# Kernel tuning notes

Measured on AMD Instinct MI355X. Metric: run time of the kernel, lower is better.

## Reference

```python
import jax, jax.numpy as jnp
import numpy as np

B = 65536
HIDDEN = 200
K = 10          # num codewords == codeword dim (NearestEmbed(k, emb_size=k))
GROUPS = HIDDEN // K  # 20 sub-vectors of dim K per sample


def setup_inputs() -> dict:
    key = jax.random.key(0)
    ks = jax.random.split(key, 10)
    s = 0.05  # small init scale
    return {
        "x": jax.random.uniform(ks[0], (B, 784), dtype=jnp.float32),
        "W1": jax.random.normal(ks[1], (400, 784), dtype=jnp.float32) * s,
        "b1": jnp.zeros((400,), dtype=jnp.float32),
        "W2": jax.random.normal(ks[2], (HIDDEN, 400), dtype=jnp.float32) * s,
        "b2": jnp.zeros((HIDDEN,), dtype=jnp.float32),
        "W3": jax.random.normal(ks[3], (400, HIDDEN), dtype=jnp.float32) * s,
        "b3": jnp.zeros((400,), dtype=jnp.float32),
        "W4": jax.random.normal(ks[4], (784, 400), dtype=jnp.float32) * s,
        "b4": jnp.zeros((784,), dtype=jnp.float32),
        "codebook": jax.random.normal(ks[5], (K, K), dtype=jnp.float32),  # (n_codes, code_dim)
    }


def _quantize(z, codebook):
    # z: (B, K, GROUPS) -- quantize each length-K column vector to nearest codeword.
    v = jnp.transpose(z, (0, 2, 1))                       # (B, G, K)
    d2 = (jnp.sum(v * v, -1, keepdims=True)
          - 2.0 * jnp.einsum('bgk,ck->bgc', v, codebook)
          + jnp.sum(codebook * codebook, -1))             # (B, G, C)
    idx = jnp.argmin(d2, axis=-1)                         # (B, G)
    q = codebook[idx]                                     # (B, G, K) gather
    return jnp.transpose(q, (0, 2, 1)), idx               # (B, K, G)


def reference(x, W1, b1, W2, b2, W3, b3, W4, b4, codebook):
    # encode
    h1 = jax.nn.relu(x @ W1.T + b1)                       # (B, 400)
    z_e_flat = h1 @ W2.T + b2                             # (B, 200)
    z_e = z_e_flat.reshape(B, K, GROUPS)                  # (B, 10, 20)

    # z_q: straight-through quantization, codebook grad stopped (weight_sg=True)
    q, _ = _quantize(z_e, codebook)
    z_q = (z_e + jax.lax.stop_gradient(q - z_e)).reshape(B, HIDDEN)

    # emb: quantize detached z_e; gradient flows only to codebook via gather
    q2, _ = _quantize(jax.lax.stop_gradient(z_e), codebook)
    emb = q2.reshape(B, HIDDEN)

    # decode (original uses tanh on the output)
    h3 = jax.nn.relu(z_q @ W3.T + b3)                     # (B, 400)
    recon = jnp.tanh(h3 @ W4.T + b4)                      # (B, 784)
    return recon, z_e, emb
```

## Files before the change

### kernel.cpp

```cpp
#include <hip/hip_runtime.h>
#include <hip/hip_bf16.h>

#define NB   65536
#define KD   10
#define NG   20
#define NH   200
#define NH1  400
#define NIN  784

#define TAU 3e-4

using short8 = __attribute__((ext_vector_type(8))) short;
using f32x4  = __attribute__((ext_vector_type(4))) float;

__device__ inline float bf2f(unsigned short u) {
  union { unsigned int i; float f; } x; x.i = ((unsigned int)u) << 16; return x.f;
}
__device__ inline unsigned short f2bf(float v) {
  __hip_bfloat16 b = __float2bfloat16(v);
  return *reinterpret_cast<unsigned short*>(&b);
}
__device__ inline void split2(float v, unsigned short& h, unsigned short& l) {
  union { float f; unsigned int i; } u; u.f = v;
  const unsigned int hbits = u.i & 0xffff0000u;
  h = (unsigned short)(hbits >> 16);
  union { unsigned int i; float f; } w; w.i = hbits;
  l = f2bf(v - w.f);
}
__device__ inline void gload_lds16(const void* g, void* l) {
  __builtin_amdgcn_global_load_lds(
      (const __attribute__((address_space(1))) unsigned int*)g,
      (__attribute__((address_space(3))) unsigned int*)l, 16, 0, 0);
}

#define KSWZ(lane) ((((lane) & 3) ^ (((lane) >> 3) & 3)) * 8)
#define CSW(lane)  (((((lane) >> 4) ^ (((lane) >> 1) & 3))) * 8)

__global__ __launch_bounds__(256) void gemm1_fused(
    const float* __restrict__ xf,
    const unsigned short* __restrict__ Bhi, const unsigned short* __restrict__ Blo,
    const float* __restrict__ bias,
    unsigned short* __restrict__ Ohi, unsigned short* __restrict__ Olo)
{
  __shared__ __align__(16) short As_hi[2][128][32];
  __shared__ __align__(16) short As_lo[2][128][32];
  __shared__ __align__(16) short Bs_hi[2][128][32];
  __shared__ __align__(16) short Bs_lo[2][128][32];
  const int tid = threadIdx.x;
  const int lane = tid & 63, wid = tid >> 6;
  const int wr = wid >> 1, wc = wid & 1;
  const int bid = blockIdx.x;
  const int sw = (bid & 7) * 256 + (bid >> 3);
  const int n0 = (sw & 3) * 128;
  const int m0 = (sw >> 2) * 128;
  const int rr = lane >> 2;
  const int kswz = KSWZ(lane);
  const int csw = CSW(lane);
  const int arow = tid >> 3;
  const int wbyte = ((tid & 7) * 8) ^ (((tid >> 4) & 3) << 4);
  const int acol = (tid & 7) * 4;

  f32x4 acc[4][4];
  #pragma unroll
  for (int i = 0; i < 4; ++i)
    #pragma unroll
    for (int j = 0; j < 4; ++j) acc[i][j] = (f32x4){0.f, 0.f, 0.f, 0.f};

  float4 va[4];

  auto loadA = [&](int ks) {
    const int k0 = ks * 32;
    #pragma unroll
    for (int p = 0; p < 4; ++p) {
      const int row = p * 32 + arow;
      const int kk = k0 + acol;
      va[p] = make_float4(0.f, 0.f, 0.f, 0.f);
      if (kk < NIN)
        va[p] = *reinterpret_cast<const float4*>(xf + (size_t)(m0 + row) * NIN + kk);
    }
  };
  auto stageB = [&](int ks, int buf) {
    const int k0 = ks * 32;
    #pragma unroll
    for (int c = 0; c < 4; ++c) {
      const int ch = wid * 4 + c;
      if (ch < 8)
        gload_lds16(Bhi + (size_t)(n0 + ch * 16 + rr) * 800 + k0 + kswz,
                    (char*)&Bs_hi[buf][0][0] + ch * 1024);
      else
        gload_lds16(Blo + (size_t)(n0 + (ch - 8) * 16 + rr) * 800 + k0 + kswz,
                    (char*)&Bs_lo[buf][0][0] + (ch - 8) * 1024);
    }
  };
  auto writeA = [&](int buf) {
    char* bh = (char*)&As_hi[buf][0][0];
    char* bl = (char*)&As_lo[buf][0][0];
    #pragma unroll
    for (int p = 0; p < 4; ++p) {
      const int row = p * 32 + arow;
      const float4 v = va[p];
      short4 h, l;
      split2(v.x, (unsigned short&)h.x, (unsigned short&)l.x);
      split2(v.y, (unsigned short&)h.y, (unsigned short&)l.y);
      split2(v.z, (unsigned short&)h.z, (unsigned short&)l.z);
      split2(v.w, (unsigned short&)h.w, (unsigned short&)l.w);
      *reinterpret_cast<short4*>(bh + row * 64 + wbyte) = h;
      *reinterpret_cast<short4*>(bl + row * 64 + wbyte) = l;
    }
  };

  loadA(0);
  stageB(0, 0);
  writeA(0);
  __syncthreads();

  for (int ks = 0; ks < 25; ++ks) {
    const int cur = ks & 1, nxt = cur ^ 1;
    const bool more = (ks + 1 < 25);
    if (more) {
      loadA(ks + 1);
      stageB(ks + 1, nxt);
    }
    short8 ah[4], al[4], bh[4], bl[4];
    #pragma unroll
    for (int i = 0; i < 4; ++i) {
      ah[i] = *reinterpret_cast<const short8*>(&As_hi[cur][wr * 64 + i * 16 + (lane & 15)][csw]);
      al[i] = *reinterpret_cast<const short8*>(&As_lo[cur][wr * 64 + i * 16 + (lane & 15)][csw]);
      bh[i] = *reinterpret_cast<const short8*>(&Bs_hi[cur][wc * 64 + i * 16 + (lane & 15)][csw]);
      bl[i] = *reinterpret_cast<const short8*>(&Bs_lo[cur][wc * 64 + i * 16 + (lane & 15)][csw]);
    }
    #pragma unroll
    for (int i = 0; i < 4; ++i)
      #pragma unroll
      for (int j = 0; j < 4; ++j) {
        acc[i][j] = __builtin_amdgcn_mfma_f32_16x16x32_bf16(ah[i], bh[j], acc[i][j], 0, 0, 0);
        acc[i][j] = __builtin_amdgcn_mfma_f32_16x16x32_bf16(al[i], bh[j], acc[i][j], 0, 0, 0);
        acc[i][j] = __builtin_amdgcn_mfma_f32_16x16x32_bf16(ah[i], bl[j], acc[i][j], 0, 0, 0);
      }
    if (more) writeA(nxt);
    __syncthreads();
  }

  #pragma unroll
  for (int j = 0; j < 4; ++j) {
    const int n = n0 + wc * 64 + j * 16 + (lane & 15);
    if (n >= NH1) continue;
    const float bn = bias[j * 0 + n];
    #pragma unroll
    for (int i = 0; i < 4; ++i) {
      const int mb = m0 + wr * 64 + i * 16 + (lane >> 4) * 4;
      #pragma unroll
      for (int r = 0; r < 4; ++r) {
        float v = fmaxf(acc[i][j][r] + bn, 0.f);
        unsigned short h, l;
        split2(v, h, l);
        Ohi[(size_t)(mb + r) * NH1 + n] = h;
        Olo[(size_t)(mb + r) * NH1 + n] = l;
      }
    }
  }
}

__global__ __launch_bounds__(256) void gemm2_split(
    const unsigned short* __restrict__ Ahi, const unsigned short* __restrict__ Alo,
    const unsigned short* __restrict__ Bhi, const unsigned short* __restrict__ Blo,
    const unsigned short* __restrict__ zp, const float* __restrict__ bias,
    float* __restrict__ Of)
{
  __shared__ __align__(16) short As_hi[128][32];
  __shared__ __align__(16) short As_lo[128][32];
  __shared__ __align__(16) short Bs_hi[128][32];
  __shared__ __align__(16) short Bs_lo[128][32];
  const int tid = threadIdx.x;
  const int lane = tid & 63, wid = tid >> 6;
  const int wr = wid >> 1, wc = wid & 1;
  const int bid = blockIdx.x;
  const int sw = (bid & 7) * 128 + (bid >> 3);
  const int n0 = (sw & 1) * 128;
  const int m0 = (sw >> 1) * 128;

  const unsigned short* G = (wid == 0) ? Ahi : (wid == 1) ? Alo
                          : (wid == 2) ? Bhi : Blo;
  short* Lt = (wid == 0) ? &As_hi[0][0] : (wid == 1) ? &As_lo[0][0]
            : (wid == 2) ? &Bs_hi[0][0] : &Bs_lo[0][0];
  const bool isA = wid < 2;
  const int rbase = isA ? m0 : n0;
  const int ld = isA ? 400 : 416;
  const int rr = lane >> 2;
  const int kswz = KSWZ(lane);
  const int csw = CSW(lane);

  f32x4 acc[4][4];
  #pragma unroll
  for (int i = 0; i < 4; ++i)
    #pragma unroll
    for (int j = 0; j < 4; ++j) acc[i][j] = (f32x4){0.f, 0.f, 0.f, 0.f};

  for (int ks = 0; ks < 13; ++ks) {
    const int k0 = ks * 32;
    #pragma unroll
    for (int c = 0; c < 8; ++c) {
      const unsigned short* src =
          G + (size_t)(rbase + c * 16 + rr) * ld + k0 + kswz;
      if (isA && (k0 + kswz >= 400)) src = zp;
      gload_lds16(src, (char*)Lt + c * 1024);
    }
    __syncthreads();
    short8 ah[4], al[4], bh[4], bl[4];
    #pragma unroll
    for (int i = 0; i < 4; ++i) {
      ah[i] = *reinterpret_cast<const short8*>(&As_hi[wr * 64 + i * 16 + (lane & 15)][csw]);
      al[i] = *reinterpret_cast<const short8*>(&As_lo[wr * 64 + i * 16 + (lane & 15)][csw]);
      bh[i] = *reinterpret_cast<const short8*>(&Bs_hi[wc * 64 + i * 16 + (lane & 15)][csw]);
      bl[i] = *reinterpret_cast<const short8*>(&Bs_lo[wc * 64 + i * 16 + (lane & 15)][csw]);
    }
    #pragma unroll
    for (int i = 0; i < 4; ++i)
      #pragma unroll
      for (int j = 0; j < 4; ++j) {
        acc[i][j] = __builtin_amdgcn_mfma_f32_16x16x32_bf16(ah[i], bh[j], acc[i][j], 0, 0, 0);
        acc[i][j] = __builtin_amdgcn_mfma_f32_16x16x32_bf16(al[i], bh[j], acc[i][j], 0, 0, 0);
        acc[i][j] = __builtin_amdgcn_mfma_f32_16x16x32_bf16(ah[i], bl[j], acc[i][j], 0, 0, 0);
      }
    __syncthreads();
  }

  #pragma unroll
  for (int j = 0; j < 4; ++j) {
    const int n = n0 + wc * 64 + j * 16 + (lane & 15);
    if (n >= NH) continue;
    const float bn = bias[n];
    #pragma unroll
    for (int i = 0; i < 4; ++i) {
      const int mb = m0 + wr * 64 + i * 16 + (lane >> 4) * 4;
      #pragma unroll
      for (int r = 0; r < 4; ++r)
        Of[(size_t)(mb + r) * NH + n] = acc[i][j][r] + bn;
    }
  }
}

__global__ __launch_bounds__(256) void gemm3_mfma(
    const unsigned short* __restrict__ A,
    const __hip_bfloat16* __restrict__ Bp,
    const float* __restrict__ bias, __hip_bfloat16* __restrict__ H3)
{
  __shared__ __align__(16) short As[128][32];
  __shared__ __align__(16) short Bs[128][32];
  const int tid = threadIdx.x;
  const int lane = tid & 63, wid = tid >> 6;
  const int wr = wid >> 1, wc = wid & 1;
  const int bid = blockIdx.x;
  const int sw = (bid & 7) * 256 + (bid >> 3);
  const int n0 = (sw & 3) * 128;
  const int m0 = (sw >> 2) * 128;
  const int kswz = KSWZ(lane);
  const int csw = CSW(lane);
  const short* Ag = (const short*)A;
  const short* Bg = (const short*)Bp;
  f32x4 acc[4][4];
  #pragma unroll
  for (int i = 0; i < 4; ++i)
    #pragma unroll
    for (int j = 0; j < 4; ++j) acc[i][j] = (f32x4){0.f, 0.f, 0.f, 0.f};

  for (int k0 = 0; k0 < 224; k0 += 32) {
    #pragma unroll
    for (int c = 0; c < 2; ++c) {
      const int row = c * 64 + wid * 16 + (lane >> 2);
      gload_lds16(Ag + (size_t)(m0 + row) * 200 + k0 + kswz,
                  (char*)&As[0][0] + c * 4096 + wid * 1024);
      gload_lds16(Bg + (size_t)(n0 + row) * 224 + k0 + kswz,
                  (char*)&Bs[0][0] + c * 4096 + wid * 1024);
    }
    __syncthreads();
    short8 af[4], bf[4];
    #pragma unroll
    for (int i = 0; i < 4; ++i)
      af[i] = *reinterpret_cast<const short8*>(&As[wr * 64 + i * 16 + (lane & 15)][csw]);
    #pragma unroll
    for (int j = 0; j < 4; ++j)
      bf[j] = *reinterpret_cast<const short8*>(&Bs[wc * 64 + j * 16 + (lane & 15)][csw]);
    #pragma unroll
    for (int i = 0; i < 4; ++i)
      #pragma unroll
      for (int j = 0; j < 4; ++j)
        acc[i][j] = __builtin_amdgcn_mfma_f32_16x16x32_bf16(af[i], bf[j], acc[i][j], 0, 0, 0);
    __syncthreads();
  }

  #pragma unroll
  for (int j = 0; j < 4; ++j) {
    const int n = n0 + wc * 64 + j * 16 + (lane & 15);
    if (n >= NH1) continue;
    const float bn = bias[n];
    #pragma unroll
    for (int i = 0; i < 4; ++i) {
      const int mb = m0 + wr * 64 + i * 16 + (lane >> 4) * 4;
      #pragma unroll
      for (int r = 0; r < 4; ++r)
        H3[(size_t)(mb + r) * NH1 + n] = __float2bfloat16(fmaxf(acc[i][j][r] + bn, 0.f));
    }
  }
}

__global__ __launch_bounds__(256) void gemm5_mfma(
    const __hip_bfloat16* __restrict__ A,
    const __hip_bfloat16* __restrict__ Bp,
    const float* __restrict__ bias, float* __restrict__ C)
{
  __shared__ __align__(16) short As[128][32];
  __shared__ __align__(16) short Bs[128][32];
  const int tid = threadIdx.x;
  const int lane = tid & 63, wid = tid >> 6;
  const int wr = wid >> 1, wc = wid & 1;
  const int bid = blockIdx.x;
  const int sw = (bid & 7) * 448 + (bid >> 3);
  const int n0 = (sw % 7) * 128;
  const int m0 = (sw / 7) * 128;
  const int kswz = KSWZ(lane);
  const int csw = CSW(lane);
  const short* Ag = (const short*)A;
  const short* Bg = (const short*)Bp;
  f32x4 acc[4][4];
  #pragma unroll
  for (int i = 0; i < 4; ++i)
    #pragma unroll
    for (int j = 0; j < 4; ++j) acc[i][j] = (f32x4){0.f, 0.f, 0.f, 0.f};

  for (int k0 = 0; k0 < 416; k0 += 32) {
    #pragma unroll
    for (int c = 0; c < 2; ++c) {
      const int row = c * 64 + wid * 16 + (lane >> 2);
      gload_lds16(Ag + (size_t)(m0 + row) * 400 + k0 + kswz,
                  (char*)&As[0][0] + c * 4096 + wid * 1024);
      gload_lds16(Bg + (size_t)(n0 + row) * 416 + k0 + kswz,
                  (char*)&Bs[0][0] + c * 4096 + wid * 1024);
    }
    __syncthreads();
    short8 af[4], bf[4];
    #pragma unroll
    for (int i = 0; i < 4; ++i)
      af[i] = *reinterpret_cast<const short8*>(&As[wr * 64 + i * 16 + (lane & 15)][csw]);
    #pragma unroll
    for (int j = 0; j < 4; ++j)
      bf[j] = *reinterpret_cast<const short8*>(&Bs[wc * 64 + j * 16 + (lane & 15)][csw]);
    #pragma unroll
    for (int i = 0; i < 4; ++i)
      #pragma unroll
      for (int j = 0; j < 4; ++j)
        acc[i][j] = __builtin_amdgcn_mfma_f32_16x16x32_bf16(af[i], bf[j], acc[i][j], 0, 0, 0);
    __syncthreads();
  }

  #pragma unroll
  for (int j = 0; j < 4; ++j) {
    const int n = n0 + wc * 64 + j * 16 + (lane & 15);
    if (n >= NIN) continue;
    const float bn = bias[n];
    #pragma unroll
    for (int i = 0; i < 4; ++i) {
      const int mb = m0 + wr * 64 + i * 16 + (lane >> 4) * 4;
      #pragma unroll
      for (int r = 0; r < 4; ++r) {
        const float zv = acc[i][j][r] + bn;
        const float t = __expf(2.0f * zv);
        C[(size_t)(mb + r) * NIN + n] = 1.0f - __fdividef(2.0f, t + 1.0f);
      }
    }
  }
}

__global__ __launch_bounds__(256) void prep_all(
    const float* __restrict__ W1, const float* __restrict__ W2,
    const float* __restrict__ W3, const float* __restrict__ W4,
    unsigned short* __restrict__ W1ph, unsigned short* __restrict__ W1pl,
    unsigned short* __restrict__ W2ph, unsigned short* __restrict__ W2pl,
    __hip_bfloat16* __restrict__ W3p, __hip_bfloat16* __restrict__ W4p)
{
  const int i = blockIdx.x * 256 + threadIdx.x;
  if (i < 409600) {
    const int n = i / 800, k = i % 800;
    const float v = (n < NH1 && k < NIN) ? W1[(size_t)n * NIN + k] : 0.f;
    unsigned short h, l; split2(v, h, l);
    W1ph[i] = h; W1pl[i] = l;
  } else if (i < 516096) {
    const int j = i - 409600;
    const int n = j / 416, k = j % 416;
    const float v = (n < NH && k < NH1) ? W2[(size_t)n * NH1 + k] : 0.f;
    unsigned short h, l; split2(v, h, l);
    W2ph[j] = h; W2pl[j] = l;
  } else if (i < 888832) {
    const int j = i - 516096;
    const int n = j / 416, k = j % 416;
    const float v = (n < NIN && k < NH1) ? W4[(size_t)n * NH1 + k] : 0.f;
    W4p[j] = __float2bfloat16(v);
  } else if (i < 1003520) {
    const int j = i - 888832;
    const int n = j / 224, k = j % 224;
    const float v = (n < NH1 && k < NH) ? W3[(size_t)n * NH + k] : 0.f;
    W3p[j] = __float2bfloat16(v);
  }
}

__global__ __launch_bounds__(256) void quant_kernel(
    const float* __restrict__ z_e, const float* __restrict__ cb,
    float* __restrict__ emb, unsigned short* __restrict__ ebf,
    unsigned char* __restrict__ sflag)
{
  __shared__ double cs[KD][KD];
  __shared__ double chalf[KD];
  __shared__ unsigned short cbf[KD][KD];
  const int tid = threadIdx.x;
  if (tid < KD * KD) {
    const double c = (double)cb[tid];
    cs[tid / KD][tid % KD] = c;
    cbf[tid / KD][tid % KD] = f2bf((float)c);
  }
  __syncthreads();
  if (tid < KD) {
    double s = 0.0;
    #pragma unroll
    for (int k = 0; k < KD; ++k) s += cs[tid][k] * cs[tid][k];
    chalf[tid] = 0.5 * s;
  }
  __syncthreads();

  const int gi = blockIdx.x * 256 + tid;
  const int b = gi / NG;
  const int g = gi % NG;
  const float* zrow = z_e + (size_t)b * NH + g;
  double v[KD];
  #pragma unroll
  for (int k = 0; k < KD; ++k) v[k] = (double)zrow[k * NG];

  int best = 0; double bt = 1e300, bt2 = 1e300;
  #pragma unroll
  for (int j = 0; j < KD; ++j) {
    double t = chalf[j];
    #pragma unroll
    for (int k = 0; k < KD; ++k) t -= v[k] * cs[j][k];
    if (t < bt) { bt2 = bt; bt = t; best = j; }
    else if (t < bt2) { bt2 = t; }
  }
  float* ep = emb + (size_t)b * NH + g;
  unsigned short* eb = ebf + (size_t)b * NH + g;
  #pragma unroll
  for (int k = 0; k < KD; ++k) {
    ep[k * NG] = (float)cs[best][k];
    eb[k * NG] = cbf[best][k];
  }
  if (bt2 - bt < TAU) sflag[b] = 1;
}

__global__ __launch_bounds__(256) void compact_kernel(
    const unsigned char* __restrict__ sflag, int* __restrict__ scount,
    int* __restrict__ slist)
{
  const int i = blockIdx.x * 256 + threadIdx.x;
  if (i < NB && sflag[i]) slist[atomicAdd(scount, 1)] = i;
}

__global__ __launch_bounds__(256) void repair_kernel(
    const float* __restrict__ x, const float* __restrict__ W1,
    const float* __restrict__ b1, const float* __restrict__ W2,
    const float* __restrict__ b2, const float* __restrict__ cb,
    const int* __restrict__ slist, const int* __restrict__ scount,
    float* __restrict__ emb, unsigned short* __restrict__ ebf)
{
  __shared__ double h1s[NH1];
  __shared__ double zs[NH];
  __shared__ double cs[KD][KD];
  __shared__ double chalf[KD];
  const int tid = threadIdx.x;
  const int lane = tid & 63, wv = tid >> 6;
  if (tid < KD * KD) cs[tid / KD][tid % KD] = (double)cb[tid];
  __syncthreads();
  if (tid < KD) {
    double s = 0.0;
    #pragma unroll
    for (int k = 0; k < KD; ++k) s += cs[tid][k] * cs[tid][k];
    chalf[tid] = 0.5 * s;
  }

  int S = *scount; if (S > NB) S = NB;

  for (int si = blockIdx.x; si < S; si += gridDim.x) {
    const int b = slist[si];
    double xr[4][4];
    #pragma unroll
    for (int it = 0; it < 4; ++it) {
      const int c4 = it * 64 + lane;
      if (c4 < 196) {
        float4 v = reinterpret_cast<const float4*>(x + (size_t)b * NIN)[c4];
        xr[it][0] = v.x; xr[it][1] = v.y; xr[it][2] = v.z; xr[it][3] = v.w;
      } else {
        xr[it][0] = xr[it][1] = xr[it][2] = xr[it][3] = 0.0;
      }
    }
    for (int j = wv; j < NH1; j += 4) {
      const float4* wr = reinterpret_cast<const float4*>(W1 + (size_t)j * NIN);
      double s0 = 0, s1 = 0, s2 = 0, s3 = 0;
      #pragma unroll
      for (int it = 0; it < 4; ++it) {
        const int c4 = it * 64 + lane;
        if (c4 < 196) {
          float4 w = wr[c4];
          s0 = fma(xr[it][0], (double)w.x, s0);
          s1 = fma(xr[it][1], (double)w.y, s1);
          s2 = fma(xr[it][2], (double)w.z, s2);
          s3 = fma(xr[it][3], (double)w.w, s3);
        }
      }
      double s = (s0 + s1) + (s2 + s3);
      #pragma unroll
      for (int off = 32; off > 0; off >>= 1) s += __shfl_down(s, off);
      if (lane == 0) { double h = s + (double)b1[j]; h1s[j] = h > 0.0 ? h : 0.0; }
    }
    __syncthreads();
    double hr[2][4];
    #pragma unroll
    for (int it = 0; it < 2; ++it) {
      const int c4 = it * 64 + lane;
      if (c4 < 100) {
        hr[it][0] = h1s[4 * c4 + 0]; hr[it][1] = h1s[4 * c4 + 1];
        hr[it][2] = h1s[4 * c4 + 2]; hr[it][3] = h1s[4 * c4 + 3];
      } else {
        hr[it][0] = hr[it][1] = hr[it][2] = hr[it][3] = 0.0;
      }
    }
    for (int n = wv; n < NH; n += 4) {
      const float4* wr = reinterpret_cast<const float4*>(W2 + (size_t)n * NH1);
      double s0 = 0, s1 = 0, s2 = 0, s3 = 0;
      #pragma unroll
      for (int it = 0; it < 2; ++it) {
        const int c4 = it * 64 + lane;
        if (c4 < 100) {
          float4 w = wr[c4];
          s0 = fma(hr[it][0], (double)w.x, s0);
          s1 = fma(hr[it][1], (double)w.y, s1);
          s2 = fma(hr[it][2], (double)w.z, s2);
          s3 = fma(hr[it][3], (double)w.w, s3);
        }
      }
      double s = (s0 + s1) + (s2 + s3);
      #pragma unroll
      for (int off = 32; off > 0; off >>= 1) s += __shfl_down(s, off);
      if (lane == 0) zs[n] = s + (double)b2[n];
    }
    __syncthreads();
    if (tid < NG) {
      const int g = tid;
      int best = 0; double bt = 1e300;
      #pragma unroll
      for (int j = 0; j < KD; ++j) {
        double t = chalf[j];
        #pragma unroll
        for (int k = 0; k < KD; ++k) t -= zs[k * NG + g] * cs[j][k];
        if (t < bt) { bt = t; best = j; }
      }
      #pragma unroll
      for (int k = 0; k < KD; ++k) {
        const float cv = (float)cs[best][k];
        emb[(size_t)b * NH + k * NG + g] = cv;
        ebf[(size_t)b * NH + k * NG + g] = f2bf(cv);
      }
    }
    __syncthreads();
  }
}

extern "C" void kernel_launch(void* const* d_in, const int* in_sizes, int n_in,
                              void* d_out, int out_size, void* d_ws, size_t ws_size,
                              hipStream_t stream) {
  const float* x  = (const float*)d_in[0];
  const float* W1 = (const float*)d_in[1];
  const float* b1 = (const float*)d_in[2];
  const float* W2 = (const float*)d_in[3];
  const float* b2 = (const float*)d_in[4];
  const float* W3 = (const float*)d_in[5];
  const float* b3 = (const float*)d_in[6];
  const float* W4 = (const float*)d_in[7];
  const float* b4 = (const float*)d_in[8];
  const float* cb = (const float*)d_in[9];

  float* out   = (float*)d_out;
  float* recon = out;
  float* z_e   = out + (size_t)NB * NIN;
  float* emb   = z_e + (size_t)NB * NH;

  unsigned short* h1_lo  = (unsigned short*)emb;
  unsigned short* emb_bf = (unsigned short*)recon;

  char* ws = (char*)d_ws;
  int*            scount = (int*)ws;
  unsigned short* zp    = (unsigned short*)(ws + 256);
  unsigned char*  sflag = (unsigned char*)(ws + 4096);
  __hip_bfloat16* W3p   = (__hip_bfloat16*)(ws + (1u << 20));
  int*            slist = (int*)(ws + (4u << 20));
  __hip_bfloat16* W4p   = (__hip_bfloat16*)(ws + (6u << 20));
  unsigned short* W1ph  = (unsigned short*)(ws + (7u << 20));
  unsigned short* W1pl  = (unsigned short*)(ws + (9u << 20));
  unsigned short* W2ph  = (unsigned short*)(ws + (11u << 20));
  unsigned short* W2pl  = (unsigned short*)(ws + (12u << 20));
  unsigned short* h1_hi = (unsigned short*)(ws + (16u << 20));
  __hip_bfloat16* h3    = (__hip_bfloat16*)(ws + (16u << 20));

  dim3 blk(256);
  hipMemsetAsync(ws, 0, 4096 + NB, stream);
  prep_all<<<3920, blk, 0, stream>>>(W1, W2, W3, W4, W1ph, W1pl, W2ph, W2pl, W3p, W4p);

  gemm1_fused<<<2048, blk, 0, stream>>>(x, W1ph, W1pl, b1, h1_hi, h1_lo);
  gemm2_split<<<1024, blk, 0, stream>>>(h1_hi, h1_lo, W2ph, W2pl, zp, b2, z_e);

  quant_kernel<<<(NB * NG) / 256, blk, 0, stream>>>(z_e, cb, emb, emb_bf, sflag);
  compact_kernel<<<NB / 256, blk, 0, stream>>>(sflag, scount, slist);
  repair_kernel<<<2048, blk, 0, stream>>>(x, W1, b1, W2, b2, cb, slist, scount, emb, emb_bf);

  gemm3_mfma<<<2048, blk, 0, stream>>>(emb_bf, W3p, b3, h3);
  gemm5_mfma<<<3584, blk, 0, stream>>>(h3, W4p, b4, recon);
}
```

Measured before the change: 595.9 us.

## Deepen GEMM software pipelines and fold row compaction into quantize kernel

gemm1 now triple-buffers the B tiles and loads them two steps ahead. It replaces __syncthreads with explicit vmcnt/lgkmcnt waits and raw barriers, so global loads overlap the MFMA work. gemm3 and gemm5 move from single-buffered LDS staging to double buffering, prefetching the next K slice while computing the current one. The separate compact kernel is removed: quant_kernel appends ambiguous rows to the repair list directly through an atomic flag exchange. This costs one launch less, but adds more LDS per block, which may lower occupancy, and relies on hand-counted wait values.

```diff
diff --git a/kernel.cpp b/kernel.cpp
--- a/kernel.cpp
+++ b/kernel.cpp
@@ -12,6 +12,10 @@
 
 using short8 = __attribute__((ext_vector_type(8))) short;
 using f32x4  = __attribute__((ext_vector_type(4))) float;
+
+#define VMCNT(n) asm volatile("s_waitcnt vmcnt(" #n ")" ::: "memory")
+#define LGKM0    asm volatile("s_waitcnt lgkmcnt(0)" ::: "memory")
+#define CFENCE   asm volatile("" ::: "memory")
 
 __device__ inline float bf2f(unsigned short u) {
   union { unsigned int i; float f; } x; x.i = ((unsigned int)u) << 16; return x.f;
@@ -44,8 +48,8 @@
 {
   __shared__ __align__(16) short As_hi[2][128][32];
   __shared__ __align__(16) short As_lo[2][128][32];
-  __shared__ __align__(16) short Bs_hi[2][128][32];
-  __shared__ __align__(16) short Bs_lo[2][128][32];
+  __shared__ __align__(16) short Bs_hi[3][128][32];
+  __shared__ __align__(16) short Bs_lo[3][128][32];
   const int tid = threadIdx.x;
   const int lane = tid & 63, wid = tid >> 6;
   const int wr = wid >> 1, wc = wid & 1;
@@ -109,25 +113,31 @@
     }
   };
 
+  stageB(0, 0);
   loadA(0);
-  stageB(0, 0);
+  CFENCE;
+  stageB(1, 1);
+  VMCNT(4);
   writeA(0);
-  __syncthreads();
+  LGKM0;
+  __builtin_amdgcn_s_barrier();
+  CFENCE;
 
   for (int ks = 0; ks < 25; ++ks) {
-    const int cur = ks & 1, nxt = cur ^ 1;
-    const bool more = (ks + 1 < 25);
-    if (more) {
-      loadA(ks + 1);
-      stageB(ks + 1, nxt);
-    }
+    const int curA = ks & 1, nxtA = curA ^ 1;
+    const int curB = ks % 3;
+    const bool moreA = (ks + 1 < 25);
+    const bool moreB = (ks + 2 < 25);
+    if (moreA) loadA(ks + 1);
+    if (moreB) stageB(ks + 2, (ks + 2) % 3);
+
     short8 ah[4], al[4], bh[4], bl[4];
     #pragma unroll
     for (int i = 0; i < 4; ++i) {
-      ah[i] = *reinterpret_cast<const short8*>(&As_hi[cur][wr * 64 + i * 16 + (lane & 15)][csw]);
-      al[i] = *reinterpret_cast<const short8*>(&As_lo[cur][wr * 64 + i * 16 + (lane & 15)][csw]);
-      bh[i] = *reinterpret_cast<const short8*>(&Bs_hi[cur][wc * 64 + i * 16 + (lane & 15)][csw]);
-      bl[i] = *reinterpret_cast<const short8*>(&Bs_lo[cur][wc * 64 + i * 16 + (lane & 15)][csw]);
+      ah[i] = *reinterpret_cast<const short8*>(&As_hi[curA][wr * 64 + i * 16 + (lane & 15)][csw]);
+      al[i] = *reinterpret_cast<const short8*>(&As_lo[curA][wr * 64 + i * 16 + (lane & 15)][csw]);
+      bh[i] = *reinterpret_cast<const short8*>(&Bs_hi[curB][wc * 64 + i * 16 + (lane & 15)][csw]);
+      bl[i] = *reinterpret_cast<const short8*>(&Bs_lo[curB][wc * 64 + i * 16 + (lane & 15)][csw]);
     }
     #pragma unroll
     for (int i = 0; i < 4; ++i)
@@ -137,15 +147,21 @@
         acc[i][j] = __builtin_amdgcn_mfma_f32_16x16x32_bf16(al[i], bh[j], acc[i][j], 0, 0, 0);
         acc[i][j] = __builtin_amdgcn_mfma_f32_16x16x32_bf16(ah[i], bl[j], acc[i][j], 0, 0, 0);
       }
-    if (more) writeA(nxt);
-    __syncthreads();
+
+    if (moreA) {
+      if (moreB) { VMCNT(4); } else { VMCNT(0); }
+      writeA(nxtA);
+      LGKM0;
+    }
+    __builtin_amdgcn_s_barrier();
+    CFENCE;
   }
 
   #pragma unroll
   for (int j = 0; j < 4; ++j) {
     const int n = n0 + wc * 64 + j * 16 + (lane & 15);
     if (n >= NH1) continue;
-    const float bn = bias[j * 0 + n];
+    const float bn = bias[n];
     #pragma unroll
     for (int i = 0; i < 4; ++i) {
       const int mb = m0 + wr * 64 + i * 16 + (lane >> 4) * 4;
@@ -245,8 +261,8 @@
     const __hip_bfloat16* __restrict__ Bp,
     const float* __restrict__ bias, __hip_bfloat16* __restrict__ H3)
 {
-  __shared__ __align__(16) short As[128][32];
-  __shared__ __align__(16) short Bs[128][32];
+  __shared__ __align__(16) short As[2][128][32];
+  __shared__ __align__(16) short Bs[2][128][32];
   const int tid = threadIdx.x;
   const int lane = tid & 63, wid = tid >> 6;
   const int wr = wid >> 1, wc = wid & 1;
@@ -264,23 +280,30 @@
     #pragma unroll
     for (int j = 0; j < 4; ++j) acc[i][j] = (f32x4){0.f, 0.f, 0.f, 0.f};
 
-  for (int k0 = 0; k0 < 224; k0 += 32) {
+  auto stage = [&](int ks, int buf) {
+    const int k0 = ks * 32;
     #pragma unroll
     for (int c = 0; c < 2; ++c) {
       const int row = c * 64 + wid * 16 + (lane >> 2);
       gload_lds16(Ag + (size_t)(m0 + row) * 200 + k0 + kswz,
-                  (char*)&As[0][0] + c * 4096 + wid * 1024);
+                  (char*)&As[buf][0][0] + c * 4096 + wid * 1024);
       gload_lds16(Bg + (size_t)(n0 + row) * 224 + k0 + kswz,
-                  (char*)&Bs[0][0] + c * 4096 + wid * 1024);
-    }
-    __syncthreads();
+                  (char*)&Bs[buf][0][0] + c * 4096 + wid * 1024);
+    }
+  };
+
+  stage(0, 0);
+  __syncthreads();
+  for (int ks = 0; ks < 7; ++ks) {
+    const int cur = ks & 1;
+    if (ks + 1 < 7) stage(ks + 1, cur ^ 1);
     short8 af[4], bf[4];
     #pragma unroll
     for (int i = 0; i < 4; ++i)
-      af[i] = *reinterpret_cast<const short8*>(&As[wr * 64 + i * 16 + (lane & 15)][csw]);
+      af[i] = *reinterpret_cast<const short8*>(&As[cur][wr * 64 + i * 16 + (lane & 15)][csw]);
     #pragma unroll
     for (int j = 0; j < 4; ++j)
-      bf[j] = *reinterpret_cast<const short8*>(&Bs[wc * 64 + j * 16 + (lane & 15)][csw]);
+      bf[j] = *reinterpret_cast<const short8*>(&Bs[cur][wc * 64 + j * 16 + (lane & 15)][csw]);
     #pragma unroll
     for (int i = 0; i < 4; ++i)
       #pragma unroll
@@ -309,8 +332,8 @@
     const __hip_bfloat16* __restrict__ Bp,
     const float* __restrict__ bias, float* __restrict__ C)
 {
-  __shared__ __align__(16) short As[128][32];
-  __shared__ __align__(16) short Bs[128][32];
+  __shared__ __align__(16) short As[2][128][32];
+  __shared__ __align__(16) short Bs[2][128][32];
   const int tid = threadIdx.x;
   const int lane = tid & 63, wid = tid >> 6;
   const int wr = wid >> 1, wc = wid & 1;
@@ -328,23 +351,30 @@
     #pragma unroll
     for (int j = 0; j < 4; ++j) acc[i][j] = (f32x4){0.f, 0.f, 0.f, 0.f};
 
-  for (int k0 = 0; k0 < 416; k0 += 32) {
+  auto stage = [&](int ks, int buf) {
+    const int k0 = ks * 32;
     #pragma unroll
     for (int c = 0; c < 2; ++c) {
       const int row = c * 64 + wid * 16 + (lane >> 2);
       gload_lds16(Ag + (size_t)(m0 + row) * 400 + k0 + kswz,
-                  (char*)&As[0][0] + c * 4096 + wid * 1024);
+                  (char*)&As[buf][0][0] + c * 4096 + wid * 1024);
       gload_lds16(Bg + (size_t)(n0 + row) * 416 + k0 + kswz,
-                  (char*)&Bs[0][0] + c * 4096 + wid * 1024);
-    }
-    __syncthreads();
+                  (char*)&Bs[buf][0][0] + c * 4096 + wid * 1024);
+    }
+  };
+
+  stage(0, 0);
+  __syncthreads();
+  for (int ks = 0; ks < 13; ++ks) {
+    const int cur = ks & 1;
+    if (ks + 1 < 13) stage(ks + 1, cur ^ 1);
     short8 af[4], bf[4];
     #pragma unroll
     for (int i = 0; i < 4; ++i)
-      af[i] = *reinterpret_cast<const short8*>(&As[wr * 64 + i * 16 + (lane & 15)][csw]);
+      af[i] = *reinterpret_cast<const short8*>(&As[cur][wr * 64 + i * 16 + (lane & 15)][csw]);
     #pragma unroll
     for (int j = 0; j < 4; ++j)
-      bf[j] = *reinterpret_cast<const short8*>(&Bs[wc * 64 + j * 16 + (lane & 15)][csw]);
+      bf[j] = *reinterpret_cast<const short8*>(&Bs[cur][wc * 64 + j * 16 + (lane & 15)][csw]);
     #pragma unroll
     for (int i = 0; i < 4; ++i)
       #pragma unroll
@@ -406,7 +436,8 @@
 __global__ __launch_bounds__(256) void quant_kernel(
     const float* __restrict__ z_e, const float* __restrict__ cb,
     float* __restrict__ emb, unsigned short* __restrict__ ebf,
-    unsigned char* __restrict__ sflag)
+    unsigned int* __restrict__ sflag, int* __restrict__ scount,
+    int* __restrict__ slist)
 {
   __shared__ double cs[KD][KD];
   __shared__ double chalf[KD];
@@ -450,15 +481,10 @@
     ep[k * NG] = (float)cs[best][k];
     eb[k * NG] = cbf[best][k];
   }
-  if (bt2 - bt < TAU) sflag[b] = 1;
-}
-
-__global__ __launch_bounds__(256) void compact_kernel(
-    const unsigned char* __restrict__ sflag, int* __restrict__ scount,
-    int* __restrict__ slist)
-{
-  const int i = blockIdx.x * 256 + threadIdx.x;
-  if (i < NB && sflag[i]) slist[atomicAdd(scount, 1)] = i;
+  if (bt2 - bt < TAU) {
+    if (atomicExch(&sflag[b], 1u) == 0u)
+      slist[atomicAdd(scount, 1)] = b;
+  }
 }
 
 __global__ __launch_bounds__(256) void repair_kernel(
@@ -595,7 +621,7 @@
   char* ws = (char*)d_ws;
   int*            scount = (int*)ws;
   unsigned short* zp    = (unsigned short*)(ws + 256);
-  unsigned char*  sflag = (unsigned char*)(ws + 4096);
+  unsigned int*   sflag = (unsigned int*)(ws + 4096);
   __hip_bfloat16* W3p   = (__hip_bfloat16*)(ws + (1u << 20));
   int*            slist = (int*)(ws + (4u << 20));
   __hip_bfloat16* W4p   = (__hip_bfloat16*)(ws + (6u << 20));
@@ -607,14 +633,13 @@
   __hip_bfloat16* h3    = (__hip_bfloat16*)(ws + (16u << 20));
 
   dim3 blk(256);
-  hipMemsetAsync(ws, 0, 4096 + NB, stream);
+  hipMemsetAsync(ws, 0, 4096 + NB * 4, stream);
   prep_all<<<3920, blk, 0, stream>>>(W1, W2, W3, W4, W1ph, W1pl, W2ph, W2pl, W3p, W4p);
 
   gemm1_fused<<<2048, blk, 0, stream>>>(x, W1ph, W1pl, b1, h1_hi, h1_lo);
   gemm2_split<<<1024, blk, 0, stream>>>(h1_hi, h1_lo, W2ph, W2pl, zp, b2, z_e);
 
-  quant_kernel<<<(NB * NG) / 256, blk, 0, stream>>>(z_e, cb, emb, emb_bf, sflag);
-  compact_kernel<<<NB / 256, blk, 0, stream>>>(sflag, scount, slist);
+  quant_kernel<<<(NB * NG) / 256, blk, 0, stream>>>(z_e, cb, emb, emb_bf, sflag, scount, slist);
   repair_kernel<<<2048, blk, 0, stream>>>(x, W1, b1, W2, b2, cb, slist, scount, emb, emb_bf);
 
   gemm3_mfma<<<2048, blk, 0, stream>>>(emb_bf, W3p, b3, h3);
```

New measurement: 674.2 us. 1.13x slower.
